# Kernel tuning notes

Hardware: AMD Instinct MI355X
Metric: run time of the kernel (lower is better)

## Reference

```python
import jax, jax.numpy as jnp
import numpy as np

OUT_FEATURES = 4096
IN_FEATURES = 4096
GROUP_SIZE = 128
N_GROUPS = OUT_FEATURES * IN_FEATURES // GROUP_SIZE  # 131072


def setup_inputs() -> dict:
    key = jax.random.key(0)
    k_x, k_t, k_s = jax.random.split(key, 3)
    x = jax.random.normal(k_x, (4, 2048, IN_FEATURES), dtype=jnp.float32)
    # ternary codes in {-1, 0, 1}, stored as int (int8 in the original module)
    ternary = jax.random.randint(k_t, (OUT_FEATURES, IN_FEATURES), 0, 3, dtype=jnp.int32) - 1
    # per-group positive scales (beta = mean |w| per group in the original init)
    scales = jax.random.uniform(k_s, (N_GROUPS,), dtype=jnp.float32, minval=0.01, maxval=0.1)
    return {"x": x, "ternary": ternary, "scales": scales}


def reference(x, ternary, scales):
    # Dequantize: expand per-group scale across group_size, multiply ternary sign.
    w = (ternary.astype(jnp.float32).reshape(-1, GROUP_SIZE) * scales[:, None])
    w = w.reshape(OUT_FEATURES, IN_FEATURES)
    # F.linear(x, W) = x @ W.T
    return jnp.einsum('bsi,oi->bso', x, w)
```

## Files before the change

kernel.cpp:

```cpp
#include <hip/hip_runtime.h>
#include <hip/hip_bf16.h>


#define Msz 8192
#define Nsz 4096
#define Ksz 4096

typedef __attribute__((ext_vector_type(8))) short short8;
typedef __attribute__((ext_vector_type(4))) float f32x4;
typedef __attribute__((ext_vector_type(4))) int int4v;
typedef __attribute__((ext_vector_type(4))) float float4v;
typedef __attribute__((ext_vector_type(8))) unsigned short ushort8;

static __device__ __forceinline__ unsigned short f2bf(float f) {
    unsigned u = __builtin_bit_cast(unsigned, f);
    u += 0x7fffu + ((u >> 16) & 1u);
    return (unsigned short)(u >> 16);
}

__global__ void prep(const float* __restrict__ x, const int* __restrict__ t,
                     const float* __restrict__ s,
                     unsigned short* __restrict__ ox, unsigned short* __restrict__ ow) {
    if (blockIdx.x < 2048) {
        int i = blockIdx.x * 256 + threadIdx.x;
        for (; i < Msz * Ksz / 8; i += 2048 * 256) {
            const float4v* p = (const float4v*)x + (size_t)i * 2;
            float4v a = p[0], b = p[1];
            ushort8 r;
            r[0] = f2bf(a[0]); r[1] = f2bf(a[1]); r[2] = f2bf(a[2]); r[3] = f2bf(a[3]);
            r[4] = f2bf(b[0]); r[5] = f2bf(b[1]); r[6] = f2bf(b[2]); r[7] = f2bf(b[3]);
            *((ushort8*)ox + i) = r;
        }
    } else {
        int i = (blockIdx.x - 2048) * 256 + threadIdx.x;
        for (; i < Nsz * Ksz / 8; i += 1024 * 256) {
            float sc = s[i >> 4];
            const int4v* p = (const int4v*)t + (size_t)i * 2;
            int4v a = p[0], b = p[1];
            ushort8 r;
            r[0] = f2bf((float)a[0] * sc); r[1] = f2bf((float)a[1] * sc);
            r[2] = f2bf((float)a[2] * sc); r[3] = f2bf((float)a[3] * sc);
            r[4] = f2bf((float)b[0] * sc); r[5] = f2bf((float)b[1] * sc);
            r[6] = f2bf((float)b[2] * sc); r[7] = f2bf((float)b[3] * sc);
            *((ushort8*)ow + i) = r;
        }
    }
}


#define DSREADS_AB(b, qm, ks) {                                                  \
    _Pragma("unroll") for (int n = 0; n < 4; ++n)                                \
      bfr[n] = *(const short8*)(L + (b)*65536 + 32768 + ((((wc)*4+n)*2+(ks))<<10) + laneA); \
    _Pragma("unroll") for (int m = 0; m < 4; ++m)                                \
      af[m] = *(const short8*)(L + (b)*65536 + ((((wr)*8+(qm)*4+m)*2+(ks))<<10) + laneA); }

#define DSREADS_A(b, qm, ks) {                                                   \
    _Pragma("unroll") for (int m = 0; m < 4; ++m)                                \
      af[m] = *(const short8*)(L + (b)*65536 + ((((wr)*8+(qm)*4+m)*2+(ks))<<10) + laneA); }

#define MFMAS(qm) {                                                              \
    _Pragma("unroll") for (int m = 0; m < 4; ++m)                                \
    _Pragma("unroll") for (int n = 0; n < 4; ++n)                                \
      acc[(qm)*4+m][n] = __builtin_amdgcn_mfma_f32_16x16x32_bf16(af[m], bfr[n], acc[(qm)*4+m][n], 0, 0, 0); }

#define STAGE(PMAT, MOFF, BOFF, T, KH) {                                         \
    _Pragma("unroll") for (int j = 0; j < 2; ++j)                                \
      __builtin_amdgcn_global_load_lds(                                          \
        (const __attribute__((address_space(1))) void*)(PMAT[j] + (T)*64 + (KH)*32), \
        (__attribute__((address_space(3))) void*)(L + (BOFF) + (MOFF) + dOff[j] + (KH)*1024), \
        16, 0, 0); }

#define STAGE_AB(BOFF, T, KH) { STAGE(pA, 0, BOFF, T, KH); STAGE(pB, 32768, BOFF, T, KH); }

#define WAITV4 asm volatile("s_waitcnt vmcnt(4)" ::: "memory");

#define PHASE(READS, QM, STG, WV)                                                \
    READS;                                                                       \
    STG;                                                                         \
    __builtin_amdgcn_sched_barrier(0);                                           \
    __builtin_amdgcn_s_barrier();                                                \
    asm volatile("s_waitcnt lgkmcnt(0)" ::: "memory");                           \
    __builtin_amdgcn_sched_barrier(0);                                           \
    __builtin_amdgcn_s_setprio(1);                                               \
    MFMAS(QM);                                                                   \
    __builtin_amdgcn_s_setprio(0);                                               \
    WV;                                                                          \
    __builtin_amdgcn_sched_barrier(0);                                           \
    __builtin_amdgcn_s_barrier();                                                \
    __builtin_amdgcn_sched_barrier(0);

__global__ __launch_bounds__(512, 2) void gemm_8p(const unsigned short* __restrict__ A,
                                                  const unsigned short* __restrict__ B,
                                                  float* __restrict__ C) {
    __shared__ __align__(16) unsigned char L[131072];

    const int tid  = threadIdx.x;
    const int lane = tid & 63;
    const int wid  = tid >> 6;
    const int wr   = wid >> 2;
    const int wc   = wid & 3;
    const int rowBase = blockIdx.y * 256;
    const int colBase = blockIdx.x * 256;

    const int laneA = (((lane & 15) * 64) + ((lane >> 4) * 16)) ^ (((lane >> 3) & 1) << 5);

    const int kloc = (lane & 1) * 8 + (((lane >> 1) ^ (lane >> 5)) & 1) * 16;
    const int r_st = lane >> 2;
    const unsigned short* pA[2];
    const unsigned short* pB[2];
    int dOff[2];
#pragma unroll
    for (int j = 0; j < 2; ++j) {
        int R = (j * 8 + wid) * 16 + r_st;
        pA[j] = A + (size_t)(rowBase + R) * Ksz + kloc;
        pB[j] = B + (size_t)(colBase + R) * Ksz + kloc;
        dOff[j] = (j * 8 + wid) * 2048;
    }

    f32x4 acc[8][4] = {};
    short8 af[4], bfr[4];

    STAGE_AB(0,     0, 0);
    STAGE_AB(0,     0, 1);
    STAGE_AB(65536, 1, 0);
    WAITV4
    __builtin_amdgcn_sched_barrier(0);
    __builtin_amdgcn_s_barrier();
    __builtin_amdgcn_sched_barrier(0);

    for (int i = 0; i < 32; ++i) {
        const int t1 = 2 * i + 1;
        const int t2 = (i < 31) ? 2 * i + 2 : 62;
        const int t3 = (i < 31) ? 2 * i + 3 : 62;

        PHASE(DSREADS_AB(0, 0, 0), 0, STAGE_AB(65536, t1, 1), )
        PHASE(DSREADS_A (0, 1, 0), 1,                       , )
        PHASE(DSREADS_AB(0, 1, 1), 1, STAGE_AB(0,     t2, 0), )
        PHASE(DSREADS_A (0, 0, 1), 0,                       , WAITV4)
        PHASE(DSREADS_AB(1, 0, 0), 0, STAGE_AB(0,     t2, 1), )
        PHASE(DSREADS_A (1, 1, 0), 1,                       , )
        PHASE(DSREADS_AB(1, 1, 1), 1, STAGE_AB(65536, t3, 0), )
        PHASE(DSREADS_A (1, 0, 1), 0,                       , WAITV4)
    }

    asm volatile("s_waitcnt vmcnt(0)" ::: "memory");

    const int crow0 = rowBase + wr * 128 + (lane >> 4) * 4;
    const int ccol0 = colBase + wc * 64 + (lane & 15);
#pragma unroll
    for (int fm = 0; fm < 8; ++fm)
#pragma unroll
        for (int fn = 0; fn < 4; ++fn) {
            float* cp = C + (size_t)(crow0 + fm * 16) * Nsz + ccol0 + fn * 16;
#pragma unroll
            for (int j = 0; j < 4; ++j)
                cp[(size_t)j * Nsz] = acc[fm][fn][j];
        }
}

__global__ void gemm_naive(const float* __restrict__ x, const int* __restrict__ t,
                           const float* __restrict__ s, float* __restrict__ C) {
    size_t o = (size_t)blockIdx.x * blockDim.x + threadIdx.x;
    if (o >= (size_t)Msz * Nsz) return;
    int m = (int)(o / Nsz), n = (int)(o % Nsz);
    float acc = 0.f;
    for (int g = 0; g < Ksz / 128; ++g) {
        float sc = s[n * (Ksz / 128) + g];
        float p = 0.f;
        const float* xp = x + (size_t)m * Ksz + g * 128;
        const int* tp = t + (size_t)n * Ksz + g * 128;
        for (int k = 0; k < 128; ++k) p += xp[k] * (float)tp[k];
        acc += sc * p;
    }
    C[o] = acc;
}

extern "C" void kernel_launch(void* const* d_in, const int* in_sizes, int n_in,
                              void* d_out, int out_size, void* d_ws, size_t ws_size,
                              hipStream_t stream) {
    const float* x      = (const float*)d_in[0];
    const int*   tern   = (const int*)d_in[1];
    const float* scales = (const float*)d_in[2];
    float* out = (float*)d_out;

    const size_t aBytes = (size_t)Msz * Ksz * 2;
    const size_t bBytes = (size_t)Nsz * Ksz * 2;

    if (ws_size >= aBytes + bBytes) {
        unsigned short* Abf = (unsigned short*)d_ws;
        unsigned short* Bbf = (unsigned short*)((char*)d_ws + aBytes);
        prep<<<3072, 256, 0, stream>>>(x, tern, scales, Abf, Bbf);
        dim3 grid(Nsz / 256, Msz / 256);
        gemm_8p<<<grid, 512, 0, stream>>>(Abf, Bbf, out);
    } else {
        gemm_naive<<<(int)(((size_t)Msz * Nsz + 255) / 256), 256, 0, stream>>>(x, tern, scales, out);
    }
}
```

Before: 284.7 us.

## Restructure GEMM pipeline into row-quarter phases with finer-grained staged loads

The main loop changes from phases split by K-half to phases split by row quarter of the A tile, with both K halves of B held in registers for the whole LDS buffer. Global-to-LDS staging is spread evenly as one half-tile load per phase, and the wait threshold moves from vmcnt(4) to vmcnt(6). The aim is to spread memory traffic evenly across phases and raise MFMA work per LDS read. In exchange, register pressure grows from the larger fragment arrays, and the LDS layout and warp-to-row mapping change.

```diff
diff --git a/kernel.cpp b/kernel.cpp
--- a/kernel.cpp
+++ b/kernel.cpp
@@ -48,31 +48,30 @@
 }
 
 
-#define DSREADS_AB(b, qm, ks) {                                                  \
+#define READ_B(b) {                                                              \
     _Pragma("unroll") for (int n = 0; n < 4; ++n)                                \
-      bfr[n] = *(const short8*)(L + (b)*65536 + 32768 + ((((wc)*4+n)*2+(ks))<<10) + laneA); \
-    _Pragma("unroll") for (int m = 0; m < 4; ++m)                                \
-      af[m] = *(const short8*)(L + (b)*65536 + ((((wr)*8+(qm)*4+m)*2+(ks))<<10) + laneA); }
+    _Pragma("unroll") for (int ks = 0; ks < 2; ++ks)                             \
+      bfr[n][ks] = *(const short8*)(L + (b)*65536 + 32768 + ((((wc)*4+n)*2+ks)<<10) + laneA); }
 
-#define DSREADS_A(b, qm, ks) {                                                   \
-    _Pragma("unroll") for (int m = 0; m < 4; ++m)                                \
-      af[m] = *(const short8*)(L + (b)*65536 + ((((wr)*8+(qm)*4+m)*2+(ks))<<10) + laneA); }
+#define READ_A(b, q) {                                                           \
+    _Pragma("unroll") for (int m = 0; m < 2; ++m)                                \
+    _Pragma("unroll") for (int ks = 0; ks < 2; ++ks)                             \
+      af[m][ks] = *(const short8*)(L + (b)*65536 + ((((q)*4+(wr)*2+m)*2+ks)<<10) + laneA); }
 
-#define MFMAS(qm) {                                                              \
-    _Pragma("unroll") for (int m = 0; m < 4; ++m)                                \
-    _Pragma("unroll") for (int n = 0; n < 4; ++n)                                \
-      acc[(qm)*4+m][n] = __builtin_amdgcn_mfma_f32_16x16x32_bf16(af[m], bfr[n], acc[(qm)*4+m][n], 0, 0, 0); }
+#define MFMAS(q) {                                                               \
+    _Pragma("unroll") for (int m = 0; m < 2; ++m)                                \
+    _Pragma("unroll") for (int n = 0; n < 4; ++n) {                              \
+      acc[(q)*2+m][n] = __builtin_amdgcn_mfma_f32_16x16x32_bf16(af[m][0], bfr[n][0], acc[(q)*2+m][n], 0, 0, 0); \
+      acc[(q)*2+m][n] = __builtin_amdgcn_mfma_f32_16x16x32_bf16(af[m][1], bfr[n][1], acc[(q)*2+m][n], 0, 0, 0); } }
 
-#define STAGE(PMAT, MOFF, BOFF, T, KH) {                                         \
+#define STAGE_H(PM, MOFF, BOFF, T, H) {                                          \
     _Pragma("unroll") for (int j = 0; j < 2; ++j)                                \
       __builtin_amdgcn_global_load_lds(                                          \
-        (const __attribute__((address_space(1))) void*)(PMAT[j] + (T)*64 + (KH)*32), \
-        (__attribute__((address_space(3))) void*)(L + (BOFF) + (MOFF) + dOff[j] + (KH)*1024), \
+        (const __attribute__((address_space(1))) void*)(PM + (size_t)((H)*128 + j*64)*Ksz + (T)*64), \
+        (__attribute__((address_space(3))) void*)(L + (BOFF) + (MOFF) + (H)*16384 + j*8192 + dOff), \
         16, 0, 0); }
 
-#define STAGE_AB(BOFF, T, KH) { STAGE(pA, 0, BOFF, T, KH); STAGE(pB, 32768, BOFF, T, KH); }
-
-#define WAITV4 asm volatile("s_waitcnt vmcnt(4)" ::: "memory");
+#define WAITV6 asm volatile("s_waitcnt vmcnt(6)" ::: "memory");
 
 #define PHASE(READS, QM, STG, WV)                                                \
     READS;                                                                       \
@@ -103,27 +102,24 @@
     const int colBase = blockIdx.x * 256;
 
     const int laneA = (((lane & 15) * 64) + ((lane >> 4) * 16)) ^ (((lane >> 3) & 1) << 5);
-
     const int kloc = (lane & 1) * 8 + (((lane >> 1) ^ (lane >> 5)) & 1) * 16;
     const int r_st = lane >> 2;
-    const unsigned short* pA[2];
-    const unsigned short* pB[2];
-    int dOff[2];
-#pragma unroll
-    for (int j = 0; j < 2; ++j) {
-        int R = (j * 8 + wid) * 16 + r_st;
-        pA[j] = A + (size_t)(rowBase + R) * Ksz + kloc;
-        pB[j] = B + (size_t)(colBase + R) * Ksz + kloc;
-        dOff[j] = (j * 8 + wid) * 2048;
-    }
+    const int dOff = wid * 1024;
+
+    const unsigned short* pAb = A + (size_t)(rowBase + (wid >> 1) * 16 + r_st) * Ksz + (wid & 1) * 32 + kloc;
+    const unsigned short* pBb = B + (size_t)(colBase + (wid >> 1) * 16 + r_st) * Ksz + (wid & 1) * 32 + kloc;
 
     f32x4 acc[8][4] = {};
-    short8 af[4], bfr[4];
+    short8 af[2][2], bfr[4][2];
 
-    STAGE_AB(0,     0, 0);
-    STAGE_AB(0,     0, 1);
-    STAGE_AB(65536, 1, 0);
-    WAITV4
+    STAGE_H(pBb, 32768, 0,     0, 0);
+    STAGE_H(pAb, 0,     0,     0, 0);
+    STAGE_H(pBb, 32768, 0,     0, 1);
+    STAGE_H(pAb, 0,     0,     0, 1);
+    STAGE_H(pBb, 32768, 65536, 1, 0);
+    STAGE_H(pAb, 0,     65536, 1, 1);
+    STAGE_H(pBb, 32768, 65536, 1, 1);
+    WAITV6
     __builtin_amdgcn_sched_barrier(0);
     __builtin_amdgcn_s_barrier();
     __builtin_amdgcn_sched_barrier(0);
@@ -133,29 +129,32 @@
         const int t2 = (i < 31) ? 2 * i + 2 : 62;
         const int t3 = (i < 31) ? 2 * i + 3 : 62;
 
-        PHASE(DSREADS_AB(0, 0, 0), 0, STAGE_AB(65536, t1, 1), )
-        PHASE(DSREADS_A (0, 1, 0), 1,                       , )
-        PHASE(DSREADS_AB(0, 1, 1), 1, STAGE_AB(0,     t2, 0), )
-        PHASE(DSREADS_A (0, 0, 1), 0,                       , WAITV4)
-        PHASE(DSREADS_AB(1, 0, 0), 0, STAGE_AB(0,     t2, 1), )
-        PHASE(DSREADS_A (1, 1, 0), 1,                       , )
-        PHASE(DSREADS_AB(1, 1, 1), 1, STAGE_AB(65536, t3, 0), )
-        PHASE(DSREADS_A (1, 0, 1), 0,                       , WAITV4)
+        PHASE({ READ_B(0); READ_A(0, 0); }, 0, STAGE_H(pAb, 0,     65536, t1, 0), )
+        PHASE(READ_A(0, 1),                 1, STAGE_H(pBb, 32768, 0,     t2, 0), )
+        PHASE(READ_A(0, 2),                 2, STAGE_H(pAb, 0,     0,     t2, 0), )
+        PHASE(READ_A(0, 3),                 3, STAGE_H(pBb, 32768, 0,     t2, 1), WAITV6)
+        PHASE({ READ_B(1); READ_A(1, 2); }, 2, STAGE_H(pAb, 0,     0,     t2, 1), )
+        PHASE(READ_A(1, 3),                 3, STAGE_H(pBb, 32768, 65536, t3, 0), )
+        PHASE(READ_A(1, 0),                 0, STAGE_H(pAb, 0,     65536, t3, 1), )
+        PHASE(READ_A(1, 1),                 1, STAGE_H(pBb, 32768, 65536, t3, 1), WAITV6)
     }
 
     asm volatile("s_waitcnt vmcnt(0)" ::: "memory");
 
-    const int crow0 = rowBase + wr * 128 + (lane >> 4) * 4;
+    const int crl = (lane >> 4) * 4;
     const int ccol0 = colBase + wc * 64 + (lane & 15);
 #pragma unroll
-    for (int fm = 0; fm < 8; ++fm)
+    for (int q = 0; q < 4; ++q)
 #pragma unroll
-        for (int fn = 0; fn < 4; ++fn) {
-            float* cp = C + (size_t)(crow0 + fm * 16) * Nsz + ccol0 + fn * 16;
+        for (int m = 0; m < 2; ++m)
 #pragma unroll
-            for (int j = 0; j < 4; ++j)
-                cp[(size_t)j * Nsz] = acc[fm][fn][j];
-        }
+            for (int n = 0; n < 4; ++n) {
+                const int row0 = rowBase + (q * 4 + wr * 2 + m) * 16 + crl;
+                float* cp = C + (size_t)row0 * Nsz + ccol0 + n * 16;
+#pragma unroll
+                for (int j = 0; j < 4; ++j)
+                    cp[(size_t)j * Nsz] = acc[q * 2 + m][n][j];
+            }
 }
 
 __global__ void gemm_naive(const float* __restrict__ x, const int* __restrict__ t,
```

Measured after the change: 266.8 us. 6.3% less time.
